# Optimization experiments

Measured on AMD Instinct MI355X. Metric: run time of the kernel, lower is better.

The kernel has to match this reference:

```python
import jax, jax.numpy as jnp
import numpy as np

ORDER = 7
ALPHA = 1.0
BETA = 1.0

def _jacobi_coeffs(order, a, b):
    k1 = np.zeros(order + 1, dtype=np.float32)
    k2 = np.zeros(order + 1, dtype=np.float32)
    k3 = np.zeros(order + 1, dtype=np.float32)
    for i in range(2, order + 1):
        k1[i] = (2*i + a + b) * (2*i + a + b - 1) / (2*i * (i + a + b))
        k2[i] = (2*i + a + b - 1) * (a*a - b*b) / (2*i * (i + a + b) * (2*i + a + b - 2))
        k3[i] = (i + a - 1) * (i + b - 1) * (2*i + a + b) / (i * (i + a + b) * (2*i + a + b - 2))
    return k1, k2, k3

K1, K2, K3 = _jacobi_coeffs(ORDER, ALPHA, BETA)

def setup_inputs() -> dict:
    key = jax.random.key(0)
    kx, kc = jax.random.split(key)
    batch, input_size, output_size = 4096, 512, 512
    x = jax.random.normal(kx, (batch, input_size), dtype=jnp.float32)
    coef = jax.random.normal(kc, (output_size, input_size, ORDER + 1), dtype=jnp.float32) * 0.1
    return {"x": x, "coef": coef}

def _precompute_jacobi(x):
    # x: [B, I] -> jacobi values [B, I, order+1]
    x = jnp.tanh(x)
    p0 = jnp.ones_like(x)
    p1 = 0.5 * (ALPHA + BETA + 2.0) * x - 0.5 * (ALPHA - BETA)
    vals = [p0, p1]
    for i in range(2, ORDER + 1):
        vals.append((K1[i] * x + K2[i]) * vals[i - 1] - K3[i] * vals[i - 2])
    return jnp.stack(vals, axis=2)  # [B, I, D]

def reference(x, coef):
    jac = _precompute_jacobi(x)                 # [B, I, D]
    # sum_j over input and order dims in one contraction
    return jnp.einsum('bid,jid->bj', jac, coef)  # [B, O]
```

## Files before the change

kernel.cpp:

```cpp
#include <hip/hip_runtime.h>
#include <stdint.h>

#define BATCH 4096
#define ISZ   512
#define OSZ   512
#define KDIM  4096

#define TM 128
#define TN 128
#define BK 64
#define SPLITK 4

typedef __bf16 bf16x8 __attribute__((ext_vector_type(8)));
typedef float  f32x4  __attribute__((ext_vector_type(4)));

__device__ __forceinline__ unsigned short f2bf(float f) {
    uint32_t u = __float_as_uint(f);
    u = (u + 0x7FFFu + ((u >> 16) & 1u)) >> 16;
    return (unsigned short)u;
}

#define NB_CONV 2048
#define NB_JAC  8192
__global__ __launch_bounds__(256) void prep(
    const float* __restrict__ coef, unsigned short* __restrict__ coefb,
    const float* __restrict__ X,    unsigned short* __restrict__ Ab)
{
    const int b = blockIdx.x;
    if (b < NB_CONV) {
        int idx = b * 256 + threadIdx.x;
        float4 v = reinterpret_cast<const float4*>(coef)[idx];
        uint2 o;
        o.x = (uint32_t)f2bf(v.x) | ((uint32_t)f2bf(v.y) << 16);
        o.y = (uint32_t)f2bf(v.z) | ((uint32_t)f2bf(v.w) << 16);
        reinterpret_cast<uint2*>(coefb)[idx] = o;
    } else {
        int idx = (b - NB_CONV) * 256 + threadIdx.x;
        float x = X[idx];
        float e  = __expf(2.0f * x);
        float t  = 1.0f - 2.0f * __builtin_amdgcn_rcpf(e + 1.0f);
        float p0 = 1.0f;
        float p1 = 2.0f * t;
        float p2 = (1.875f     * t) * p1 - 0.75f       * p0;
        float p3 = (1.8666667f * t) * p2 - 0.8f        * p1;
        float p4 = (1.875f     * t) * p3 - 0.83333333f * p2;
        float p5 = (1.8857143f * t) * p4 - 0.85714287f * p3;
        float p6 = (1.8958333f * t) * p5 - 0.875f      * p4;
        float p7 = (1.9047619f * t) * p6 - 0.88888889f * p5;
        uint4 o;
        o.x = (uint32_t)f2bf(p0) | ((uint32_t)f2bf(p1) << 16);
        o.y = (uint32_t)f2bf(p2) | ((uint32_t)f2bf(p3) << 16);
        o.z = (uint32_t)f2bf(p4) | ((uint32_t)f2bf(p5) << 16);
        o.w = (uint32_t)f2bf(p6) | ((uint32_t)f2bf(p7) << 16);
        reinterpret_cast<uint4*>(Ab)[idx] = o;
    }
}

__global__ __launch_bounds__(256, 2) void gemm_fused(
    const unsigned short* __restrict__ Am,
    const unsigned short* __restrict__ Bm,
    unsigned short* __restrict__ Cp,
    int M, int N, int K)
{
    __shared__ __align__(16) unsigned short As[2][TM * BK];
    __shared__ __align__(16) unsigned short Bs[2][TN * BK];

    const int tid  = threadIdx.x;
    const int wave = tid >> 6;
    const int lane = tid & 63;
    const int wm   = (wave >> 1) * 64;
    const int wn   = (wave & 1) * 64;

    const size_t baseA = (size_t)blockIdx.x * TM * K;
    const size_t baseB = (size_t)blockIdx.y * TN * K;
    const int kper  = K / SPLITK;
    const int kbeg  = blockIdx.z * kper;
    const int niter = kper / BK;

    f32x4 acc[4][4] = {};

    const int mrow = lane & 15;
    const int kc   = lane >> 4;

    auto stage = [&](const unsigned short* __restrict__ G, size_t gbase,
                     unsigned short* lds, int k0) {
        #pragma unroll
        for (int it = 0; it < 4; ++it) {
            int s    = it * 256 + tid;
            int row  = s >> 3;
            int csrc = (s & 7) ^ (row & 7);
            const unsigned short* g = G + gbase + (size_t)row * K + k0 + csrc * 8;
            unsigned short* l = lds + (size_t)(it * 256 + wave * 64) * 8;
            __builtin_amdgcn_global_load_lds(
                (const __attribute__((address_space(1))) uint32_t*)g,
                (__attribute__((address_space(3))) uint32_t*)l, 16, 0, 0);
        }
    };

    stage(Bm, baseB, &Bs[0][0], kbeg);
    stage(Am, baseA, &As[0][0], kbeg);
    __syncthreads();

    for (int kt = 0; kt < niter; ++kt) {
        const int k0 = kbeg + kt * BK;
        const int p  = kt & 1;
        if (kt + 1 < niter) {
            stage(Bm, baseB, &Bs[1 - p][0], k0 + BK);
            stage(Am, baseA, &As[1 - p][0], k0 + BK);
        }

        const unsigned short* Ap = &As[p][0];
        const unsigned short* Bp = &Bs[p][0];
        #pragma unroll
        for (int ks = 0; ks < BK; ks += 32) {
            bf16x8 aF[4], bF[4];
            const int cbase = (ks >> 3) + kc;
            #pragma unroll
            for (int mi = 0; mi < 4; ++mi) {
                int r = wm + mi * 16 + mrow;
                int slot = r * 8 + (cbase ^ (r & 7));
                aF[mi] = *reinterpret_cast<const bf16x8*>(Ap + (size_t)slot * 8);
            }
            #pragma unroll
            for (int ni = 0; ni < 4; ++ni) {
                int r = wn + ni * 16 + mrow;
                int slot = r * 8 + (cbase ^ (r & 7));
                bF[ni] = *reinterpret_cast<const bf16x8*>(Bp + (size_t)slot * 8);
            }
            #pragma unroll
            for (int mi = 0; mi < 4; ++mi)
                #pragma unroll
                for (int ni = 0; ni < 4; ++ni)
                    acc[mi][ni] = __builtin_amdgcn_mfma_f32_16x16x32_bf16(
                        aF[mi], bF[ni], acc[mi][ni], 0, 0, 0);
        }
        __syncthreads();
    }

    unsigned short* Cz = Cp + (size_t)blockIdx.z * M * N;
    const int orow = blockIdx.x * TM + wm + (lane >> 4) * 4;
    const int ocol = blockIdx.y * TN + wn + (lane & 15);
    #pragma unroll
    for (int mi = 0; mi < 4; ++mi)
        #pragma unroll
        for (int ni = 0; ni < 4; ++ni)
            #pragma unroll
            for (int r = 0; r < 4; ++r)
                Cz[(size_t)(orow + mi * 16 + r) * N + ocol + ni * 16] =
                    f2bf(acc[mi][ni][r]);
}

__global__ __launch_bounds__(256) void reduce_k(
    const unsigned short* __restrict__ part, float* __restrict__ out, int n8)
{
    int idx = blockIdx.x * 256 + threadIdx.x;
    if (idx >= n8) return;
    const uint4* p = reinterpret_cast<const uint4*>(part);
    float s[8] = {};
    #pragma unroll
    for (int z = 0; z < SPLITK; ++z) {
        uint4 v = p[(size_t)z * n8 + idx];
        s[0] += __uint_as_float((v.x & 0xFFFFu) << 16);
        s[1] += __uint_as_float(v.x & 0xFFFF0000u);
        s[2] += __uint_as_float((v.y & 0xFFFFu) << 16);
        s[3] += __uint_as_float(v.y & 0xFFFF0000u);
        s[4] += __uint_as_float((v.z & 0xFFFFu) << 16);
        s[5] += __uint_as_float(v.z & 0xFFFF0000u);
        s[6] += __uint_as_float((v.w & 0xFFFFu) << 16);
        s[7] += __uint_as_float(v.w & 0xFFFF0000u);
    }
    float4 o0 = {s[0], s[1], s[2], s[3]};
    float4 o1 = {s[4], s[5], s[6], s[7]};
    reinterpret_cast<float4*>(out)[2 * idx]     = o0;
    reinterpret_cast<float4*>(out)[2 * idx + 1] = o1;
}

extern "C" void kernel_launch(void* const* d_in, const int* in_sizes, int n_in,
                              void* d_out, int out_size, void* d_ws, size_t ws_size,
                              hipStream_t stream)
{
    const float* x    = (const float*)d_in[0];
    const float* coef = (const float*)d_in[1];
    float* out = (float*)d_out;

    unsigned short* part  = (unsigned short*)d_ws;
    unsigned short* coefb = part  + (size_t)SPLITK * BATCH * OSZ;
    unsigned short* Ab    = coefb + (size_t)OSZ * KDIM;

    prep<<<NB_CONV + NB_JAC, 256, 0, stream>>>(coef, coefb, x, Ab);

    dim3 grid(BATCH / TM, OSZ / TN, SPLITK);
    gemm_fused<<<grid, 256, 0, stream>>>(Ab, coefb, part, BATCH, OSZ, KDIM);

    int n8r = (BATCH * OSZ) / 8;
    reduce_k<<<(n8r + 255) / 256, 256, 0, stream>>>(part, out, n8r);
}
```

Measured before the change: 96.02 us.

## Rewrite GEMM as 256x256 tile, 8-wave, 4-stage pipelined kernel with split-K 8

Replaces the 128x128 double-buffered GEMM with a 512-thread kernel. Each block computes a 256x256 tile over a 4-deep LDS ring with BK=32. Global-to-LDS loads are interleaved with MFMA phases using explicit vmcnt waits, sched barriers and s_setprio, and the 1D grid is remapped so nearby workgroups share operands. Split-K rises to 8 so the 256 blocks fill the device, and the Jacobi prep kernel now handles four inputs per thread with vectorized loads. The trade-off is twice as many bf16 partial outputs for the reduce kernel to read back, plus much higher LDS use per block.

```diff
diff --git a/kernel.cpp b/kernel.cpp
--- a/kernel.cpp
+++ b/kernel.cpp
@@ -6,10 +6,12 @@
 #define OSZ   512
 #define KDIM  4096
 
-#define TM 128
-#define TN 128
-#define BK 64
-#define SPLITK 4
+#define BM 256
+#define BN 256
+#define BK 32
+#define SPLITK 8
+#define KPER (KDIM / SPLITK)
+#define NT   (KPER / BK)
 
 typedef __bf16 bf16x8 __attribute__((ext_vector_type(8)));
 typedef float  f32x4  __attribute__((ext_vector_type(4)));
@@ -21,7 +23,7 @@
 }
 
 #define NB_CONV 2048
-#define NB_JAC  8192
+#define NB_JAC  2048
 __global__ __launch_bounds__(256) void prep(
     const float* __restrict__ coef, unsigned short* __restrict__ coefb,
     const float* __restrict__ X,    unsigned short* __restrict__ Ab)
@@ -36,112 +38,161 @@
         reinterpret_cast<uint2*>(coefb)[idx] = o;
     } else {
         int idx = (b - NB_CONV) * 256 + threadIdx.x;
-        float x = X[idx];
-        float e  = __expf(2.0f * x);
-        float t  = 1.0f - 2.0f * __builtin_amdgcn_rcpf(e + 1.0f);
-        float p0 = 1.0f;
-        float p1 = 2.0f * t;
-        float p2 = (1.875f     * t) * p1 - 0.75f       * p0;
-        float p3 = (1.8666667f * t) * p2 - 0.8f        * p1;
-        float p4 = (1.875f     * t) * p3 - 0.83333333f * p2;
-        float p5 = (1.8857143f * t) * p4 - 0.85714287f * p3;
-        float p6 = (1.8958333f * t) * p5 - 0.875f      * p4;
-        float p7 = (1.9047619f * t) * p6 - 0.88888889f * p5;
-        uint4 o;
-        o.x = (uint32_t)f2bf(p0) | ((uint32_t)f2bf(p1) << 16);
-        o.y = (uint32_t)f2bf(p2) | ((uint32_t)f2bf(p3) << 16);
-        o.z = (uint32_t)f2bf(p4) | ((uint32_t)f2bf(p5) << 16);
-        o.w = (uint32_t)f2bf(p6) | ((uint32_t)f2bf(p7) << 16);
-        reinterpret_cast<uint4*>(Ab)[idx] = o;
-    }
-}
-
-__global__ __launch_bounds__(256, 2) void gemm_fused(
+        float4 xv = reinterpret_cast<const float4*>(X)[idx];
+        const float xs[4] = {xv.x, xv.y, xv.z, xv.w};
+        #pragma unroll
+        for (int j = 0; j < 4; ++j) {
+            float e  = __expf(2.0f * xs[j]);
+            float t  = 1.0f - 2.0f * __builtin_amdgcn_rcpf(e + 1.0f);
+            float p0 = 1.0f;
+            float p1 = 2.0f * t;
+            float p2 = (1.875f     * t) * p1 - 0.75f       * p0;
+            float p3 = (1.8666667f * t) * p2 - 0.8f        * p1;
+            float p4 = (1.875f     * t) * p3 - 0.83333333f * p2;
+            float p5 = (1.8857143f * t) * p4 - 0.85714287f * p3;
+            float p6 = (1.8958333f * t) * p5 - 0.875f      * p4;
+            float p7 = (1.9047619f * t) * p6 - 0.88888889f * p5;
+            uint4 o;
+            o.x = (uint32_t)f2bf(p0) | ((uint32_t)f2bf(p1) << 16);
+            o.y = (uint32_t)f2bf(p2) | ((uint32_t)f2bf(p3) << 16);
+            o.z = (uint32_t)f2bf(p4) | ((uint32_t)f2bf(p5) << 16);
+            o.w = (uint32_t)f2bf(p6) | ((uint32_t)f2bf(p7) << 16);
+            reinterpret_cast<uint4*>(Ab)[idx * 4 + j] = o;
+        }
+    }
+}
+
+#define SB __builtin_amdgcn_sched_barrier(0)
+#define VM8 asm volatile("s_waitcnt vmcnt(8)" ::: "memory")
+#define VM0 asm volatile("s_waitcnt vmcnt(0)" ::: "memory")
+
+__global__ __launch_bounds__(512, 2) void gemm_8p(
     const unsigned short* __restrict__ Am,
     const unsigned short* __restrict__ Bm,
     unsigned short* __restrict__ Cp,
     int M, int N, int K)
 {
-    __shared__ __align__(16) unsigned short As[2][TM * BK];
-    __shared__ __align__(16) unsigned short Bs[2][TN * BK];
+    __shared__ __align__(16) unsigned short As[4][BM * BK];
+    __shared__ __align__(16) unsigned short Bs[4][BN * BK];
 
     const int tid  = threadIdx.x;
     const int wave = tid >> 6;
     const int lane = tid & 63;
-    const int wm   = (wave >> 1) * 64;
-    const int wn   = (wave & 1) * 64;
-
-    const size_t baseA = (size_t)blockIdx.x * TM * K;
-    const size_t baseB = (size_t)blockIdx.y * TN * K;
-    const int kper  = K / SPLITK;
-    const int kbeg  = blockIdx.z * kper;
-    const int niter = kper / BK;
-
-    f32x4 acc[4][4] = {};
-
+    const int wm   = (wave >> 2) * 128;
+    const int wn   = (wave & 3) * 64;
     const int mrow = lane & 15;
     const int kc   = lane >> 4;
 
-    auto stage = [&](const unsigned short* __restrict__ G, size_t gbase,
-                     unsigned short* lds, int k0) {
-        #pragma unroll
-        for (int it = 0; it < 4; ++it) {
-            int s    = it * 256 + tid;
-            int row  = s >> 3;
-            int csrc = (s & 7) ^ (row & 7);
-            const unsigned short* g = G + gbase + (size_t)row * K + k0 + csrc * 8;
-            unsigned short* l = lds + (size_t)(it * 256 + wave * 64) * 8;
+    const int wg  = blockIdx.x;
+    const int swz = (wg & 7) * 32 + (wg >> 3);
+    const int z   = swz >> 5;
+    const int rr  = swz & 31;
+    const int by  = rr >> 4;
+    const int bx  = rr & 15;
+
+    const size_t baseA = (size_t)bx * BM * K;
+    const size_t baseB = (size_t)by * BN * K;
+    const int kbeg = z * KPER;
+
+    f32x4 acc[8][4] = {};
+
+    int aoff[8], boff[4];
+    #pragma unroll
+    for (int mi = 0; mi < 8; ++mi) {
+        int r = wm + mi * 16 + mrow, g = r >> 1;
+        aoff[mi] = (g * 8 + ((((r & 1) << 2) + kc) ^ (g & 7))) * 8;
+    }
+    #pragma unroll
+    for (int ni = 0; ni < 4; ++ni) {
+        int r = wn + ni * 16 + mrow, g = r >> 1;
+        boff[ni] = (g * 8 + ((((r & 1) << 2) + kc) ^ (g & 7))) * 8;
+    }
+    int sOff[2];
+    #pragma unroll
+    for (int it = 0; it < 2; ++it) {
+        int s = it * 512 + tid;
+        int g = s >> 3, cc = (s & 7) ^ (g & 7);
+        sOff[it] = (2 * g + (cc >> 2)) * K + (cc & 3) * 8;
+    }
+
+    auto stageA = [&](int tt) {
+        unsigned short* dst = &As[tt & 3][0];
+        const unsigned short* src = Am + baseA + kbeg + tt * BK;
+        #pragma unroll
+        for (int it = 0; it < 2; ++it)
             __builtin_amdgcn_global_load_lds(
-                (const __attribute__((address_space(1))) uint32_t*)g,
-                (__attribute__((address_space(3))) uint32_t*)l, 16, 0, 0);
-        }
+                (const __attribute__((address_space(1))) uint32_t*)(src + sOff[it]),
+                (__attribute__((address_space(3))) uint32_t*)
+                    (dst + (size_t)(it * 512 + wave * 64) * 8), 16, 0, 0);
     };
-
-    stage(Bm, baseB, &Bs[0][0], kbeg);
-    stage(Am, baseA, &As[0][0], kbeg);
-    __syncthreads();
-
-    for (int kt = 0; kt < niter; ++kt) {
-        const int k0 = kbeg + kt * BK;
-        const int p  = kt & 1;
-        if (kt + 1 < niter) {
-            stage(Bm, baseB, &Bs[1 - p][0], k0 + BK);
-            stage(Am, baseA, &As[1 - p][0], k0 + BK);
-        }
-
-        const unsigned short* Ap = &As[p][0];
-        const unsigned short* Bp = &Bs[p][0];
-        #pragma unroll
-        for (int ks = 0; ks < BK; ks += 32) {
-            bf16x8 aF[4], bF[4];
-            const int cbase = (ks >> 3) + kc;
-            #pragma unroll
-            for (int mi = 0; mi < 4; ++mi) {
-                int r = wm + mi * 16 + mrow;
-                int slot = r * 8 + (cbase ^ (r & 7));
-                aF[mi] = *reinterpret_cast<const bf16x8*>(Ap + (size_t)slot * 8);
-            }
-            #pragma unroll
-            for (int ni = 0; ni < 4; ++ni) {
-                int r = wn + ni * 16 + mrow;
-                int slot = r * 8 + (cbase ^ (r & 7));
-                bF[ni] = *reinterpret_cast<const bf16x8*>(Bp + (size_t)slot * 8);
-            }
-            #pragma unroll
-            for (int mi = 0; mi < 4; ++mi)
-                #pragma unroll
-                for (int ni = 0; ni < 4; ++ni)
-                    acc[mi][ni] = __builtin_amdgcn_mfma_f32_16x16x32_bf16(
-                        aF[mi], bF[ni], acc[mi][ni], 0, 0, 0);
-        }
-        __syncthreads();
-    }
-
-    unsigned short* Cz = Cp + (size_t)blockIdx.z * M * N;
-    const int orow = blockIdx.x * TM + wm + (lane >> 4) * 4;
-    const int ocol = blockIdx.y * TN + wn + (lane & 15);
-    #pragma unroll
-    for (int mi = 0; mi < 4; ++mi)
+    auto stageB = [&](int tt) {
+        unsigned short* dst = &Bs[tt & 3][0];
+        const unsigned short* src = Bm + baseB + kbeg + tt * BK;
+        #pragma unroll
+        for (int it = 0; it < 2; ++it)
+            __builtin_amdgcn_global_load_lds(
+                (const __attribute__((address_space(1))) uint32_t*)(src + sOff[it]),
+                (__attribute__((address_space(3))) uint32_t*)
+                    (dst + (size_t)(it * 512 + wave * 64) * 8), 16, 0, 0);
+    };
+
+#define KTILE(T, STG, WAITSTMT)                                            \
+  {                                                                        \
+    const unsigned short* Ap = &As[(T) & 3][0];                            \
+    const unsigned short* Bp = &Bs[(T) & 3][0];                            \
+    bf16x8 aF[4], bF[4];                                                   \
+    SB;                                                                    \
+    _Pragma("unroll")                                                      \
+    for (int mi = 0; mi < 4; ++mi)                                         \
+      aF[mi] = *reinterpret_cast<const bf16x8*>(Ap + aoff[mi]);            \
+    _Pragma("unroll")                                                      \
+    for (int ni = 0; ni < 4; ++ni)                                         \
+      bF[ni] = *reinterpret_cast<const bf16x8*>(Bp + boff[ni]);            \
+    if (STG) stageA((T) + 3);                                              \
+    SB; __builtin_amdgcn_s_barrier(); SB;                                  \
+    __builtin_amdgcn_s_setprio(1);                                         \
+    _Pragma("unroll")                                                      \
+    for (int mi = 0; mi < 4; ++mi)                                         \
+      _Pragma("unroll")                                                    \
+      for (int ni = 0; ni < 4; ++ni)                                       \
+        acc[mi][ni] = __builtin_amdgcn_mfma_f32_16x16x32_bf16(             \
+            aF[mi], bF[ni], acc[mi][ni], 0, 0, 0);                         \
+    __builtin_amdgcn_s_setprio(0);                                         \
+    SB; __builtin_amdgcn_s_barrier();                                      \
+    SB;                                                                    \
+    _Pragma("unroll")                                                      \
+    for (int mi = 0; mi < 4; ++mi)                                         \
+      aF[mi] = *reinterpret_cast<const bf16x8*>(Ap + aoff[4 + mi]);        \
+    if (STG) stageB((T) + 3);                                              \
+    SB; __builtin_amdgcn_s_barrier(); SB;                                  \
+    __builtin_amdgcn_s_setprio(1);                                         \
+    _Pragma("unroll")                                                      \
+    for (int mi = 0; mi < 4; ++mi)                                         \
+      _Pragma("unroll")                                                    \
+      for (int ni = 0; ni < 4; ++ni)                                       \
+        acc[4 + mi][ni] = __builtin_amdgcn_mfma_f32_16x16x32_bf16(         \
+            aF[mi], bF[ni], acc[4 + mi][ni], 0, 0, 0);                     \
+    __builtin_amdgcn_s_setprio(0);                                         \
+    SB; WAITSTMT; __builtin_amdgcn_s_barrier();                            \
+  }
+
+    stageA(0); stageB(0);
+    stageA(1); stageB(1);
+    stageA(2); stageB(2);
+    VM8;
+    __builtin_amdgcn_s_barrier();
+
+    for (int t = 0; t < NT - 3; ++t)
+        KTILE(t, true, VM8);
+    KTILE(NT - 3, false, VM0);
+    KTILE(NT - 2, false, VM0);
+    KTILE(NT - 1, false, VM0);
+
+    unsigned short* Cz = Cp + (size_t)z * M * N;
+    const int orow = bx * BM + wm + (lane >> 4) * 4;
+    const int ocol = by * BN + wn + (lane & 15);
+    #pragma unroll
+    for (int mi = 0; mi < 8; ++mi)
         #pragma unroll
         for (int ni = 0; ni < 4; ++ni)
             #pragma unroll
@@ -189,8 +240,7 @@
 
     prep<<<NB_CONV + NB_JAC, 256, 0, stream>>>(coef, coefb, x, Ab);
 
-    dim3 grid(BATCH / TM, OSZ / TN, SPLITK);
-    gemm_fused<<<grid, 256, 0, stream>>>(Ab, coefb, part, BATCH, OSZ, KDIM);
+    gemm_8p<<<256, 512, 0, stream>>>(Ab, coefb, part, BATCH, OSZ, KDIM);
 
     int n8r = (BATCH * OSZ) / 8;
     reduce_k<<<(n8r + 255) / 256, 256, 0, stream>>>(part, out, n8r);
```

Measured after the change: 108.6 us. 13.1% more time.

## Rewrite GEMM with 256x128 tiles, triple-buffered LDS, and interleaved MFMA/load schedule

Applied to the files above, without the earlier changes.

The GEMM moves to 512-thread blocks with 256x128 tiles and a three-slot LDS ring. Each tile is split into two MFMA halves, and the next tile's register fragments are preloaded between them, coordinated by explicit vmcnt waits, barriers and setprio. Workgroup IDs are remapped (XCD-aware swizzle) into a 1D grid, and the prep kernel now computes 4 Jacobi elements per thread from float4 loads. The intent is to hide global and LDS latency and raise MFMA utilization, at the cost of fragile hand scheduling and more LDS per block.

```diff
diff --git a/kernel.cpp b/kernel.cpp
--- a/kernel.cpp
+++ b/kernel.cpp
@@ -6,10 +6,12 @@
 #define OSZ   512
 #define KDIM  4096
 
-#define TM 128
-#define TN 128
+#define BM 256
+#define BN 128
 #define BK 64
 #define SPLITK 4
+#define KPER (KDIM / SPLITK)
+#define NT   (KPER / BK)
 
 typedef __bf16 bf16x8 __attribute__((ext_vector_type(8)));
 typedef float  f32x4  __attribute__((ext_vector_type(4)));
@@ -21,7 +23,7 @@
 }
 
 #define NB_CONV 2048
-#define NB_JAC  8192
+#define NB_JAC  2048
 __global__ __launch_bounds__(256) void prep(
     const float* __restrict__ coef, unsigned short* __restrict__ coefb,
     const float* __restrict__ X,    unsigned short* __restrict__ Ab)
@@ -36,110 +38,184 @@
         reinterpret_cast<uint2*>(coefb)[idx] = o;
     } else {
         int idx = (b - NB_CONV) * 256 + threadIdx.x;
-        float x = X[idx];
-        float e  = __expf(2.0f * x);
-        float t  = 1.0f - 2.0f * __builtin_amdgcn_rcpf(e + 1.0f);
-        float p0 = 1.0f;
-        float p1 = 2.0f * t;
-        float p2 = (1.875f     * t) * p1 - 0.75f       * p0;
-        float p3 = (1.8666667f * t) * p2 - 0.8f        * p1;
-        float p4 = (1.875f     * t) * p3 - 0.83333333f * p2;
-        float p5 = (1.8857143f * t) * p4 - 0.85714287f * p3;
-        float p6 = (1.8958333f * t) * p5 - 0.875f      * p4;
-        float p7 = (1.9047619f * t) * p6 - 0.88888889f * p5;
-        uint4 o;
-        o.x = (uint32_t)f2bf(p0) | ((uint32_t)f2bf(p1) << 16);
-        o.y = (uint32_t)f2bf(p2) | ((uint32_t)f2bf(p3) << 16);
-        o.z = (uint32_t)f2bf(p4) | ((uint32_t)f2bf(p5) << 16);
-        o.w = (uint32_t)f2bf(p6) | ((uint32_t)f2bf(p7) << 16);
-        reinterpret_cast<uint4*>(Ab)[idx] = o;
-    }
-}
-
-__global__ __launch_bounds__(256, 2) void gemm_fused(
+        float4 xv = reinterpret_cast<const float4*>(X)[idx];
+        const float xs[4] = {xv.x, xv.y, xv.z, xv.w};
+        #pragma unroll
+        for (int j = 0; j < 4; ++j) {
+            float e  = __expf(2.0f * xs[j]);
+            float t  = 1.0f - 2.0f * __builtin_amdgcn_rcpf(e + 1.0f);
+            float p0 = 1.0f;
+            float p1 = 2.0f * t;
+            float p2 = (1.875f     * t) * p1 - 0.75f       * p0;
+            float p3 = (1.8666667f * t) * p2 - 0.8f        * p1;
+            float p4 = (1.875f     * t) * p3 - 0.83333333f * p2;
+            float p5 = (1.8857143f * t) * p4 - 0.85714287f * p3;
+            float p6 = (1.8958333f * t) * p5 - 0.875f      * p4;
+            float p7 = (1.9047619f * t) * p6 - 0.88888889f * p5;
+            uint4 o;
+            o.x = (uint32_t)f2bf(p0) | ((uint32_t)f2bf(p1) << 16);
+            o.y = (uint32_t)f2bf(p2) | ((uint32_t)f2bf(p3) << 16);
+            o.z = (uint32_t)f2bf(p4) | ((uint32_t)f2bf(p5) << 16);
+            o.w = (uint32_t)f2bf(p6) | ((uint32_t)f2bf(p7) << 16);
+            reinterpret_cast<uint4*>(Ab)[idx * 4 + j] = o;
+        }
+    }
+}
+
+#define SB  __builtin_amdgcn_sched_barrier(0)
+#define BAR __builtin_amdgcn_s_barrier()
+#define VM6 asm volatile("s_waitcnt vmcnt(6)" ::: "memory")
+#define VM0 asm volatile("s_waitcnt vmcnt(0)" ::: "memory")
+
+__global__ __launch_bounds__(512, 2) void gemm_p(
     const unsigned short* __restrict__ Am,
     const unsigned short* __restrict__ Bm,
     unsigned short* __restrict__ Cp,
     int M, int N, int K)
 {
-    __shared__ __align__(16) unsigned short As[2][TM * BK];
-    __shared__ __align__(16) unsigned short Bs[2][TN * BK];
+    __shared__ __align__(16) unsigned short As[3][BM * BK];
+    __shared__ __align__(16) unsigned short Bs[3][BN * BK];
 
     const int tid  = threadIdx.x;
     const int wave = tid >> 6;
     const int lane = tid & 63;
     const int wm   = (wave >> 1) * 64;
     const int wn   = (wave & 1) * 64;
-
-    const size_t baseA = (size_t)blockIdx.x * TM * K;
-    const size_t baseB = (size_t)blockIdx.y * TN * K;
-    const int kper  = K / SPLITK;
-    const int kbeg  = blockIdx.z * kper;
-    const int niter = kper / BK;
-
-    f32x4 acc[4][4] = {};
-
     const int mrow = lane & 15;
     const int kc   = lane >> 4;
 
-    auto stage = [&](const unsigned short* __restrict__ G, size_t gbase,
-                     unsigned short* lds, int k0) {
-        #pragma unroll
-        for (int it = 0; it < 4; ++it) {
-            int s    = it * 256 + tid;
-            int row  = s >> 3;
-            int csrc = (s & 7) ^ (row & 7);
-            const unsigned short* g = G + gbase + (size_t)row * K + k0 + csrc * 8;
-            unsigned short* l = lds + (size_t)(it * 256 + wave * 64) * 8;
+    const int wg = blockIdx.x;
+    const int gx = (wg & 7) * 32 + (wg >> 3);
+    const int by = gx & 3;
+    const int bx = (gx >> 2) & 15;
+    const int z  = gx >> 6;
+
+    const size_t baseA = (size_t)bx * BM * K;
+    const size_t baseB = (size_t)by * BN * K;
+    const int kbeg = z * KPER;
+
+    f32x4 acc[4][4] = {};
+    bf16x8 a01[2][2], a23[2][2];
+    bf16x8 bqP[4][2], bqQ[4][2];
+
+    int aoff[4][2], boff[4][2];
+    #pragma unroll
+    for (int mi = 0; mi < 4; ++mi)
+        #pragma unroll
+        for (int kk = 0; kk < 2; ++kk) {
+            int r = wm + mi * 16 + mrow;
+            aoff[mi][kk] = (r * 8 + ((kk * 4 + kc) ^ (r & 7))) * 8;
+        }
+    #pragma unroll
+    for (int ni = 0; ni < 4; ++ni)
+        #pragma unroll
+        for (int kk = 0; kk < 2; ++kk) {
+            int r = wn + ni * 16 + mrow;
+            boff[ni][kk] = (r * 8 + ((kk * 4 + kc) ^ (r & 7))) * 8;
+        }
+    int sOffA[4], sOffB[2];
+    #pragma unroll
+    for (int it = 0; it < 4; ++it) {
+        int s = it * 512 + tid, row = s >> 3, c = (s & 7) ^ (row & 7);
+        sOffA[it] = row * K + c * 8;
+    }
+    #pragma unroll
+    for (int it = 0; it < 2; ++it) {
+        int s = it * 512 + tid, row = s >> 3, c = (s & 7) ^ (row & 7);
+        sOffB[it] = row * K + c * 8;
+    }
+
+    auto stageT = [&](int t, int slot) {
+        const unsigned short* sa = Am + baseA + kbeg + t * BK;
+        unsigned short* da = &As[slot][0];
+        #pragma unroll
+        for (int it = 0; it < 4; ++it)
             __builtin_amdgcn_global_load_lds(
-                (const __attribute__((address_space(1))) uint32_t*)g,
-                (__attribute__((address_space(3))) uint32_t*)l, 16, 0, 0);
-        }
-    };
-
-    stage(Bm, baseB, &Bs[0][0], kbeg);
-    stage(Am, baseA, &As[0][0], kbeg);
-    __syncthreads();
-
-    for (int kt = 0; kt < niter; ++kt) {
-        const int k0 = kbeg + kt * BK;
-        const int p  = kt & 1;
-        if (kt + 1 < niter) {
-            stage(Bm, baseB, &Bs[1 - p][0], k0 + BK);
-            stage(Am, baseA, &As[1 - p][0], k0 + BK);
-        }
-
-        const unsigned short* Ap = &As[p][0];
-        const unsigned short* Bp = &Bs[p][0];
-        #pragma unroll
-        for (int ks = 0; ks < BK; ks += 32) {
-            bf16x8 aF[4], bF[4];
-            const int cbase = (ks >> 3) + kc;
-            #pragma unroll
-            for (int mi = 0; mi < 4; ++mi) {
-                int r = wm + mi * 16 + mrow;
-                int slot = r * 8 + (cbase ^ (r & 7));
-                aF[mi] = *reinterpret_cast<const bf16x8*>(Ap + (size_t)slot * 8);
-            }
-            #pragma unroll
-            for (int ni = 0; ni < 4; ++ni) {
-                int r = wn + ni * 16 + mrow;
-                int slot = r * 8 + (cbase ^ (r & 7));
-                bF[ni] = *reinterpret_cast<const bf16x8*>(Bp + (size_t)slot * 8);
-            }
-            #pragma unroll
-            for (int mi = 0; mi < 4; ++mi)
+                (const __attribute__((address_space(1))) uint32_t*)(sa + sOffA[it]),
+                (__attribute__((address_space(3))) uint32_t*)
+                    (da + (size_t)(it * 512 + wave * 64) * 8), 16, 0, 0);
+        const unsigned short* sb = Bm + baseB + kbeg + t * BK;
+        unsigned short* db = &Bs[slot][0];
+        #pragma unroll
+        for (int it = 0; it < 2; ++it)
+            __builtin_amdgcn_global_load_lds(
+                (const __attribute__((address_space(1))) uint32_t*)(sb + sOffB[it]),
+                (__attribute__((address_space(3))) uint32_t*)
+                    (db + (size_t)(it * 512 + wave * 64) * 8), 16, 0, 0);
+    };
+    auto rdA01 = [&](const unsigned short* Ap) {
+        #pragma unroll
+        for (int m2 = 0; m2 < 2; ++m2)
+            #pragma unroll
+            for (int kk = 0; kk < 2; ++kk)
+                a01[m2][kk] = *reinterpret_cast<const bf16x8*>(Ap + aoff[m2][kk]);
+    };
+    auto rdA23 = [&](const unsigned short* Ap) {
+        #pragma unroll
+        for (int m2 = 0; m2 < 2; ++m2)
+            #pragma unroll
+            for (int kk = 0; kk < 2; ++kk)
+                a23[m2][kk] = *reinterpret_cast<const bf16x8*>(Ap + aoff[2 + m2][kk]);
+    };
+    auto rdB = [&](bf16x8 (&dst)[4][2], const unsigned short* Bp) {
+        #pragma unroll
+        for (int ni = 0; ni < 4; ++ni)
+            #pragma unroll
+            for (int kk = 0; kk < 2; ++kk)
+                dst[ni][kk] = *reinterpret_cast<const bf16x8*>(Bp + boff[ni][kk]);
+    };
+
+    auto tileBody = [&](int t, bf16x8 (&BQC)[4][2], bf16x8 (&BQN)[4][2],
+                        const unsigned short* Ap, const unsigned short* Apn,
+                        const unsigned short* Bpn, int stageSlot) {
+        if (t < NT - 2) stageT(t + 2, stageSlot);
+        rdA23(Ap);
+        SB; BAR; SB;
+        __builtin_amdgcn_s_setprio(1);
+        #pragma unroll
+        for (int m2 = 0; m2 < 2; ++m2)
+            #pragma unroll
+            for (int ni = 0; ni < 4; ++ni)
                 #pragma unroll
-                for (int ni = 0; ni < 4; ++ni)
-                    acc[mi][ni] = __builtin_amdgcn_mfma_f32_16x16x32_bf16(
-                        aF[mi], bF[ni], acc[mi][ni], 0, 0, 0);
-        }
-        __syncthreads();
-    }
-
-    unsigned short* Cz = Cp + (size_t)blockIdx.z * M * N;
-    const int orow = blockIdx.x * TM + wm + (lane >> 4) * 4;
-    const int ocol = blockIdx.y * TN + wn + (lane & 15);
+                for (int kk = 0; kk < 2; ++kk)
+                    acc[m2][ni] = __builtin_amdgcn_mfma_f32_16x16x32_bf16(
+                        a01[m2][kk], BQC[ni][kk], acc[m2][ni], 0, 0, 0);
+        __builtin_amdgcn_s_setprio(0);
+        SB;
+        if (t < NT - 2) { VM6; } else if (t == NT - 2) { VM0; }
+        BAR; SB;
+        if (t < NT - 1) { rdA01(Apn); rdB(BQN, Bpn); }
+        SB; BAR; SB;
+        __builtin_amdgcn_s_setprio(1);
+        #pragma unroll
+        for (int m2 = 0; m2 < 2; ++m2)
+            #pragma unroll
+            for (int ni = 0; ni < 4; ++ni)
+                #pragma unroll
+                for (int kk = 0; kk < 2; ++kk)
+                    acc[2 + m2][ni] = __builtin_amdgcn_mfma_f32_16x16x32_bf16(
+                        a23[m2][kk], BQC[ni][kk], acc[2 + m2][ni], 0, 0, 0);
+        __builtin_amdgcn_s_setprio(0);
+        SB; BAR;
+    };
+
+    stageT(0, 0);
+    stageT(1, 1);
+    VM6;
+    BAR;
+    rdA01(&As[0][0]);
+    rdB(bqP, &Bs[0][0]);
+
+    int s0 = 0, s1 = 1, s2 = 2;
+    for (int t = 0; t < NT; t += 2) {
+        tileBody(t,     bqP, bqQ, &As[s0][0], &As[s1][0], &Bs[s1][0], s2);
+        tileBody(t + 1, bqQ, bqP, &As[s1][0], &As[s2][0], &Bs[s2][0], s0);
+        int tmp = s0; s0 = s2; s2 = s1; s1 = tmp;
+    }
+
+    unsigned short* Cz = Cp + (size_t)z * M * N;
+    const int orow = bx * BM + wm + (lane >> 4) * 4;
+    const int ocol = by * BN + wn + (lane & 15);
     #pragma unroll
     for (int mi = 0; mi < 4; ++mi)
         #pragma unroll
@@ -189,8 +265,7 @@
 
     prep<<<NB_CONV + NB_JAC, 256, 0, stream>>>(coef, coefb, x, Ab);
 
-    dim3 grid(BATCH / TM, OSZ / TN, SPLITK);
-    gemm_fused<<<grid, 256, 0, stream>>>(Ab, coefb, part, BATCH, OSZ, KDIM);
+    gemm_p<<<256, 512, 0, stream>>>(Ab, coefb, part, BATCH, OSZ, KDIM);
 
     int n8r = (BATCH * OSZ) / 8;
     reduce_k<<<(n8r + 255) / 256, 256, 0, stream>>>(part, out, n8r);
```

After: 104.5 us. 8.8% more time.
